# Kernel tuning notes

Measured on AMD Instinct MI355X. Metric: run time of the kernel, lower is better.

Reference implementation:

```python
import jax, jax.numpy as jnp
import numpy as np

N_NODES = 50000
TAU = 1.0 + (1.0 / 1000.0) * (0.1 - 1.0)  # anneal step 1 -> 0.9991


def setup_inputs() -> dict:
    key = jax.random.key(0)
    ks = jax.random.split(key, 8)
    N, F, H, E, K = N_NODES, 128, 128, 800000, 5
    node_features = jax.random.normal(ks[0], (N, F), dtype=jnp.float32)
    src = jnp.sort(jax.random.randint(ks[1], (E,), 0, N, dtype=jnp.int32))
    dst = jax.random.randint(ks[2], (E,), 0, N, dtype=jnp.int32)
    u_noise = jax.random.uniform(ks[3], (K, E), dtype=jnp.float32,
                                 minval=1e-6, maxval=1.0 - 1e-6)
    # MLP params: Linear(2F -> H), ReLU, Linear(H -> 1)
    W1 = jax.random.normal(ks[4], (2 * F, H), dtype=jnp.float32) / np.sqrt(2 * F)
    b1 = jnp.zeros((H,), dtype=jnp.float32)
    W2 = jax.random.normal(ks[5], (H, 1), dtype=jnp.float32) / np.sqrt(H)
    b2 = jnp.zeros((1,), dtype=jnp.float32)
    return {"node_features": node_features, "W1": W1, "b1": b1,
            "W2": W2, "b2": b2, "u_noise": u_noise, "src": src, "dst": dst}


def reference(node_features, W1, b1, W2, b2, u_noise, src, dst):
    N = N_NODES
    F = node_features.shape[1]
    # per-edge MLP on concat([x_u, x_v]) without materializing the (E, 2F) concat
    x_u = node_features[src]                      # (E, F)
    x_v = node_features[dst]                      # (E, F)
    h = jax.nn.relu(x_u @ W1[:F] + x_v @ W1[F:] + b1)   # (E, H)
    z = (h @ W2 + b2)[:, 0]                       # (E,)
    # per-node (segment) log-softmax over each node's neighbor edges
    zmax = jax.ops.segment_max(z, src, num_segments=N)
    ze = z - zmax[src]
    denom = jax.ops.segment_sum(jnp.exp(ze), src, num_segments=N)
    log_pi = ze - jnp.log(denom)[src]             # (E,)
    # k rounds of Gumbel-softmax sampling
    g = -jnp.log(-jnp.log(u_noise))               # (K, E)
    scores = (log_pi[None, :] + g) / TAU          # (K, E)

    def seg_softmax(s):
        m = jax.ops.segment_max(s, src, num_segments=N)
        e = jnp.exp(s - m[src])
        return e / jax.ops.segment_sum(e, src, num_segments=N)[src]

    def seg_argmax_dst(s):
        m = jax.ops.segment_max(s, src, num_segments=N)
        hit = s >= m[src]
        sel = jax.ops.segment_max(jnp.where(hit, dst, -1), src, num_segments=N)
        return sel  # (N,) selected neighbor per node, per round

    soft = jax.vmap(seg_softmax)(scores)          # (K, E) gumbel-softmax probs
    selected = jax.vmap(seg_argmax_dst)(scores)   # (K, N) sampled neighbor ids
    return selected, soft
```

## Files before the change

### kernel.cpp

```cpp
#include <hip/hip_runtime.h>

#define FEAT 128
#define HID  128
#define XS_S 260

__global__ __launch_bounds__(256) void gemm_ab(
    const float* __restrict__ X, const float* __restrict__ W1,
    float* __restrict__ A, float* __restrict__ B, int N) {
  __shared__ float xs[32 * XS_S];
  const int t = threadIdx.x;
  const int lane = t & 63;
  const int n0 = blockIdx.x * 256;
  const int j0 = blockIdx.y * 64;
  const int jj = __builtin_amdgcn_readfirstlane(j0 + (t >> 6) * 16);
  const float* Wp = W1 + (jj < 128 ? jj : 128 * HID + (jj - 128));
  float* Obase = (jj < 128) ? (A + jj) : (B + (jj - 128));

  const int ln = t >> 3;
  const int lf = (t & 7) * 4;

  float acc[4][16];
#pragma unroll
  for (int r = 0; r < 4; ++r)
#pragma unroll
    for (int c = 0; c < 16; ++c) acc[r][c] = 0.f;

  for (int kc = 0; kc < 4; ++kc) {
    __syncthreads();
#pragma unroll
    for (int rep = 0; rep < 8; ++rep) {
      const int nl = ln + rep * 32;
      const int n = n0 + nl;
      float4 v = make_float4(0.f, 0.f, 0.f, 0.f);
      if (n < N) v = *(const float4*)(X + (size_t)n * FEAT + kc * 32 + lf);
      xs[(lf + 0) * XS_S + nl] = v.x;
      xs[(lf + 1) * XS_S + nl] = v.y;
      xs[(lf + 2) * XS_S + nl] = v.z;
      xs[(lf + 3) * XS_S + nl] = v.w;
    }
    __syncthreads();

#pragma unroll 4
    for (int k = 0; k < 32; ++k) {
      const float* wr = Wp + (size_t)(kc * 32 + k) * HID;
      const float4 w0 = *(const float4*)(wr);
      const float4 w1 = *(const float4*)(wr + 4);
      const float4 w2 = *(const float4*)(wr + 8);
      const float4 w3 = *(const float4*)(wr + 12);
      const float4 xv = *(const float4*)&xs[k * XS_S + lane * 4];
      const float xr[4] = {xv.x, xv.y, xv.z, xv.w};
      const float wv[16] = {w0.x, w0.y, w0.z, w0.w, w1.x, w1.y, w1.z, w1.w,
                            w2.x, w2.y, w2.z, w2.w, w3.x, w3.y, w3.z, w3.w};
#pragma unroll
      for (int r = 0; r < 4; ++r)
#pragma unroll
        for (int c = 0; c < 16; ++c)
          acc[r][c] = fmaf(xr[r], wv[c], acc[r][c]);
    }
  }

#pragma unroll
  for (int r = 0; r < 4; ++r) {
    const int n = n0 + lane * 4 + r;
    if (n < N) {
      float* o = Obase + (size_t)n * HID;
#pragma unroll
      for (int c4 = 0; c4 < 4; ++c4)
        *(float4*)(o + c4 * 4) = make_float4(acc[r][c4 * 4 + 0], acc[r][c4 * 4 + 1],
                                             acc[r][c4 * 4 + 2], acc[r][c4 * 4 + 3]);
    }
  }
}

__global__ __launch_bounds__(256) void row_offsets(
    const int* __restrict__ src, int* __restrict__ rs, int N, int E) {
  const int n = blockIdx.x * 256 + threadIdx.x;
  if (n > N) return;
  int lo = 0, hi = E;
  while (lo < hi) {
    const int mid = (lo + hi) >> 1;
    if (src[mid] < n) lo = mid + 1; else hi = mid;
  }
  rs[n] = lo;
}

struct Rows { float4 a0, a1, b0, b1, c0, c1, d0, d1; };

__device__ __forceinline__ void load_pair(
    const float* __restrict__ A, const float* __restrict__ B,
    const int* __restrict__ src, const int* __restrict__ dst,
    int e0, int E, int l, Rows& r) {
  const bool k0 = e0 < E, k1 = e0 + 1 < E;
  const int u0 = k0 ? src[e0] : 0;
  const int v0 = k0 ? dst[e0] : 0;
  const int u1 = k1 ? src[e0 + 1] : 0;
  const int v1 = k1 ? dst[e0 + 1] : 0;
  const float4* Au0 = (const float4*)(A + (size_t)u0 * HID) + l * 2;
  const float4* Bv0 = (const float4*)(B + (size_t)v0 * HID) + l * 2;
  const float4* Au1 = (const float4*)(A + (size_t)u1 * HID) + l * 2;
  const float4* Bv1 = (const float4*)(B + (size_t)v1 * HID) + l * 2;
  r.a0 = Au0[0]; r.a1 = Au0[1];
  r.b0 = Bv0[0]; r.b1 = Bv0[1];
  r.c0 = Au1[0]; r.c1 = Au1[1];
  r.d0 = Bv1[0]; r.d1 = Bv1[1];
}

__global__ __launch_bounds__(256) void edge_z(
    const float* __restrict__ A, const float* __restrict__ B,
    const float* __restrict__ b1, const float* __restrict__ W2,
    const float* __restrict__ b2, const int* __restrict__ src,
    const int* __restrict__ dst, float* __restrict__ z, int E) {
  const int g = threadIdx.x >> 4;
  const int l = threadIdx.x & 15;
  const int base = blockIdx.x * 128 + g * 2;

  const float4 c0 = *(const float4*)(b1 + l * 8);
  const float4 c1 = *(const float4*)(b1 + l * 8 + 4);
  const float4 w0 = *(const float4*)(W2 + l * 8);
  const float4 w1 = *(const float4*)(W2 + l * 8 + 4);
  const float bias2 = b2[0];

  Rows cur, nxt;
  load_pair(A, B, src, dst, base, E, l, cur);

#pragma unroll 4
  for (int it = 0; it < 4; ++it) {
    const int e0 = base + it * 32;
    if (it < 3) load_pair(A, B, src, dst, base + (it + 1) * 32, E, l, nxt);

    float p0 = fmaxf(cur.a0.x + cur.b0.x + c0.x, 0.f) * w0.x
             + fmaxf(cur.a0.y + cur.b0.y + c0.y, 0.f) * w0.y
             + fmaxf(cur.a0.z + cur.b0.z + c0.z, 0.f) * w0.z
             + fmaxf(cur.a0.w + cur.b0.w + c0.w, 0.f) * w0.w
             + fmaxf(cur.a1.x + cur.b1.x + c1.x, 0.f) * w1.x
             + fmaxf(cur.a1.y + cur.b1.y + c1.y, 0.f) * w1.y
             + fmaxf(cur.a1.z + cur.b1.z + c1.z, 0.f) * w1.z
             + fmaxf(cur.a1.w + cur.b1.w + c1.w, 0.f) * w1.w;
    float p1 = fmaxf(cur.c0.x + cur.d0.x + c0.x, 0.f) * w0.x
             + fmaxf(cur.c0.y + cur.d0.y + c0.y, 0.f) * w0.y
             + fmaxf(cur.c0.z + cur.d0.z + c0.z, 0.f) * w0.z
             + fmaxf(cur.c0.w + cur.d0.w + c0.w, 0.f) * w0.w
             + fmaxf(cur.c1.x + cur.d1.x + c1.x, 0.f) * w1.x
             + fmaxf(cur.c1.y + cur.d1.y + c1.y, 0.f) * w1.y
             + fmaxf(cur.c1.z + cur.d1.z + c1.z, 0.f) * w1.z
             + fmaxf(cur.c1.w + cur.d1.w + c1.w, 0.f) * w1.w;

#pragma unroll
    for (int m = 8; m >= 1; m >>= 1) {
      p0 += __shfl_xor(p0, m);
      p1 += __shfl_xor(p1, m);
    }
    if (l == 0 && e0 < E) {
      z[e0] = p0 + bias2;
      if (e0 + 1 < E) z[e0 + 1] = p1 + bias2;
    }
    cur = nxt;
  }
}

__global__ __launch_bounds__(256) void seg_sample(
    const float* __restrict__ z, const float* __restrict__ U,
    const int* __restrict__ dst, const int* __restrict__ rs,
    float* __restrict__ out_sel, float* __restrict__ out_soft,
    int N, int E, int K) {
  const int t = threadIdx.x;
  const int lane = t & 63;
  const int half = lane >> 5;
  const int hl = lane & 31;
  const int n = blockIdx.x * 8 + (t >> 6) * 2 + half;
  const float INVTAU = 1.0f / 0.9991f;

  int start = 0, deg = 0;
  if (n < N) { start = rs[n]; deg = rs[n + 1] - start; }

  if (__all(deg <= 32)) {
    if (n >= N) return;
    if (deg == 0) {
      if (hl == 0)
        for (int k = 0; k < K; ++k) out_sel[(size_t)k * N + n] = -2147483648.0f;
      return;
    }
    const bool act = hl < deg;
    const int e = start + (act ? hl : 0);
    const float zv = act ? z[e] : -INFINITY;
    const int d = act ? dst[e] : -1;

    float zmax = zv;
#pragma unroll
    for (int m = 16; m >= 1; m >>= 1) zmax = fmaxf(zmax, __shfl_xor(zmax, m));
    float den = act ? __expf(zv - zmax) : 0.f;
#pragma unroll
    for (int m = 16; m >= 1; m >>= 1) den += __shfl_xor(den, m);
    const float lpb = (zv - zmax) - __logf(den);

    for (int k = 0; k < K; ++k) {
      float ex = 0.f;
      if (act) {
        const float uu = U[(size_t)k * E + e];
        const float t2 = -__logf(uu);
        const float g = -__logf(t2);
        ex = __expf((lpb + g) * INVTAU);
      }
      float d2 = ex;
      float mx = ex;
      int md = d;
#pragma unroll
      for (int m = 16; m >= 1; m >>= 1) {
        d2 += __shfl_xor(d2, m);
        const float ox = __shfl_xor(mx, m);
        const int od = __shfl_xor(md, m);
        if (ox > mx) { mx = ox; md = od; }
        else if (ox == mx) md = max(md, od);
      }
      if (hl == 0) out_sel[(size_t)k * N + n] = (float)md;
      if (act) {
        const float inv = __builtin_amdgcn_rcpf(d2);
        out_soft[(size_t)k * E + e] = ex * inv;
      }
    }
    return;
  }

  const int wbase = blockIdx.x * 8 + (t >> 6) * 2;
  for (int j = 0; j < 2; ++j) {
    const int nn = wbase + j;
    if (nn >= N) continue;
    const int st = rs[nn];
    const int dg = rs[nn + 1] - st;
    if (dg == 0) {
      if (lane == 0)
        for (int k = 0; k < K; ++k) out_sel[(size_t)k * N + nn] = -2147483648.0f;
      continue;
    }
    float zmax = -INFINITY;
    for (int c = lane; c < dg; c += 64) zmax = fmaxf(zmax, z[st + c]);
#pragma unroll
    for (int m = 32; m >= 1; m >>= 1) zmax = fmaxf(zmax, __shfl_xor(zmax, m));
    float den = 0.f;
    for (int c = lane; c < dg; c += 64) den += expf(z[st + c] - zmax);
#pragma unroll
    for (int m = 32; m >= 1; m >>= 1) den += __shfl_xor(den, m);
    const float logd = logf(den);

    for (int k = 0; k < K; ++k) {
      float m2 = -INFINITY;
      for (int c = lane; c < dg; c += 64) {
        const int e = st + c;
        const float g = -logf(-logf(U[(size_t)k * E + e]));
        const float s = ((z[e] - zmax) - logd + g) * INVTAU;
        m2 = fmaxf(m2, s);
      }
#pragma unroll
      for (int m = 32; m >= 1; m >>= 1) m2 = fmaxf(m2, __shfl_xor(m2, m));
      float d2 = 0.f;
      int cand = -1;
      for (int c = lane; c < dg; c += 64) {
        const int e = st + c;
        const float g = -logf(-logf(U[(size_t)k * E + e]));
        const float s = ((z[e] - zmax) - logd + g) * INVTAU;
        d2 += expf(s - m2);
        if (s >= m2) cand = max(cand, dst[e]);
      }
#pragma unroll
      for (int m = 32; m >= 1; m >>= 1) d2 += __shfl_xor(d2, m);
#pragma unroll
      for (int m = 32; m >= 1; m >>= 1) cand = max(cand, __shfl_xor(cand, m));
      if (lane == 0) out_sel[(size_t)k * N + nn] = (float)cand;
      for (int c = lane; c < dg; c += 64) {
        const int e = st + c;
        const float g = -logf(-logf(U[(size_t)k * E + e]));
        const float s = ((z[e] - zmax) - logd + g) * INVTAU;
        out_soft[(size_t)k * E + e] = expf(s - m2) / d2;
      }
    }
  }
}

extern "C" void kernel_launch(void* const* d_in, const int* in_sizes, int n_in,
                              void* d_out, int out_size, void* d_ws, size_t ws_size,
                              hipStream_t stream) {
  const float* X  = (const float*)d_in[0];
  const float* W1 = (const float*)d_in[1];
  const float* b1 = (const float*)d_in[2];
  const float* W2 = (const float*)d_in[3];
  const float* b2 = (const float*)d_in[4];
  const float* U  = (const float*)d_in[5];
  const int* src  = (const int*)d_in[6];
  const int* dst  = (const int*)d_in[7];
  const int E = in_sizes[6];
  const int K = in_sizes[5] / E;
  const int N = in_sizes[0] / FEAT;

  float* A = (float*)d_ws;
  float* B = A + (size_t)N * HID;
  float* z = B + (size_t)N * HID;
  int* rs  = (int*)(z + E);

  float* out_sel  = (float*)d_out;
  float* out_soft = (float*)d_out + (size_t)K * N;

  hipLaunchKernelGGL(gemm_ab, dim3((N + 255) / 256, 4), dim3(256), 0, stream,
                     X, W1, A, B, N);
  hipLaunchKernelGGL(row_offsets, dim3((N + 256) / 256), dim3(256), 0, stream,
                     src, rs, N, E);
  hipLaunchKernelGGL(edge_z, dim3((E + 127) / 128), dim3(256), 0, stream,
                     A, B, b1, W2, b2, src, dst, z, E);
  hipLaunchKernelGGL(seg_sample, dim3((N + 7) / 8), dim3(256), 0, stream,
                     z, U, dst, rs, out_sel, out_soft, N, E, K);
}
```

Before: 246.0 us.

## Stage W1 tiles in shared memory and compute full 256-column output per block

The node GEMM now has each block cover 128 nodes and all 256 output columns (both the A and B halves) instead of one 64-column slice per block. W1 chunks are staged into padded shared memory rather than read by each wave straight from global memory. Each thread now accumulates an 8x16 register tile instead of 4x16, raising arithmetic intensity, and X is read once rather than four times. In exchange it uses more registers and LDS, which may lower occupancy, and the grid becomes smaller.

```diff
diff --git a/kernel.cpp b/kernel.cpp
--- a/kernel.cpp
+++ b/kernel.cpp
@@ -2,33 +2,40 @@
 
 #define FEAT 128
 #define HID  128
-#define XS_S 260
+#define XS_S 132
+#define WS_S 320
 
 __global__ __launch_bounds__(256) void gemm_ab(
     const float* __restrict__ X, const float* __restrict__ W1,
     float* __restrict__ A, float* __restrict__ B, int N) {
   __shared__ float xs[32 * XS_S];
+  __shared__ float ws[32 * WS_S];
   const int t = threadIdx.x;
+  const int n0 = blockIdx.x * 128;
+
+  const int wave = t >> 6;
+  const int wc = wave & 1;
+  const int wn = wave >> 1;
   const int lane = t & 63;
-  const int n0 = blockIdx.x * 256;
-  const int j0 = blockIdx.y * 64;
-  const int jj = __builtin_amdgcn_readfirstlane(j0 + (t >> 6) * 16);
-  const float* Wp = W1 + (jj < 128 ? jj : 128 * HID + (jj - 128));
-  float* Obase = (jj < 128) ? (A + jj) : (B + (jj - 128));
+  const int ng = lane >> 3;
+  const int cg = lane & 7;
+  const int xbase = wn * 64 + ng * 8;
+  const int cb = wc * 128 + cg * 16;
+  const int woff = cb + ((cb >> 4) << 2);
 
   const int ln = t >> 3;
   const int lf = (t & 7) * 4;
 
-  float acc[4][16];
-#pragma unroll
-  for (int r = 0; r < 4; ++r)
+  float acc[8][16];
+#pragma unroll
+  for (int r = 0; r < 8; ++r)
 #pragma unroll
     for (int c = 0; c < 16; ++c) acc[r][c] = 0.f;
 
   for (int kc = 0; kc < 4; ++kc) {
     __syncthreads();
 #pragma unroll
-    for (int rep = 0; rep < 8; ++rep) {
+    for (int rep = 0; rep < 4; ++rep) {
       const int nl = ln + rep * 32;
       const int n = n0 + nl;
       float4 v = make_float4(0.f, 0.f, 0.f, 0.f);
@@ -38,32 +45,46 @@
       xs[(lf + 2) * XS_S + nl] = v.z;
       xs[(lf + 3) * XS_S + nl] = v.w;
     }
+#pragma unroll
+    for (int rep = 0; rep < 8; ++rep) {
+      const int idx = rep * 256 + t;
+      const int k = idx >> 6;
+      const int jc = (idx & 63) * 4;
+      const float* srcp = (jc < 128)
+          ? W1 + (size_t)(kc * 32 + k) * HID + jc
+          : W1 + (size_t)(128 + kc * 32 + k) * HID + (jc - 128);
+      *(float4*)&ws[k * WS_S + jc + ((jc >> 4) << 2)] = *(const float4*)srcp;
+    }
     __syncthreads();
 
-#pragma unroll 4
+#pragma unroll 2
     for (int k = 0; k < 32; ++k) {
-      const float* wr = Wp + (size_t)(kc * 32 + k) * HID;
+      const float* wr = &ws[k * WS_S + woff];
       const float4 w0 = *(const float4*)(wr);
       const float4 w1 = *(const float4*)(wr + 4);
       const float4 w2 = *(const float4*)(wr + 8);
       const float4 w3 = *(const float4*)(wr + 12);
-      const float4 xv = *(const float4*)&xs[k * XS_S + lane * 4];
-      const float xr[4] = {xv.x, xv.y, xv.z, xv.w};
+      const float* xr = &xs[k * XS_S + xbase];
+      const float4 x0 = *(const float4*)(xr);
+      const float4 x1 = *(const float4*)(xr + 4);
+      const float xv[8] = {x0.x, x0.y, x0.z, x0.w, x1.x, x1.y, x1.z, x1.w};
       const float wv[16] = {w0.x, w0.y, w0.z, w0.w, w1.x, w1.y, w1.z, w1.w,
                             w2.x, w2.y, w2.z, w2.w, w3.x, w3.y, w3.z, w3.w};
 #pragma unroll
-      for (int r = 0; r < 4; ++r)
+      for (int r = 0; r < 8; ++r)
 #pragma unroll
         for (int c = 0; c < 16; ++c)
-          acc[r][c] = fmaf(xr[r], wv[c], acc[r][c]);
-    }
-  }
-
-#pragma unroll
-  for (int r = 0; r < 4; ++r) {
-    const int n = n0 + lane * 4 + r;
+          acc[r][c] = fmaf(xv[r], wv[c], acc[r][c]);
+    }
+  }
+
+  float* Obase = (cb < 128) ? A : B;
+  const int cbm = (cb < 128) ? cb : cb - 128;
+#pragma unroll
+  for (int r = 0; r < 8; ++r) {
+    const int n = n0 + xbase + r;
     if (n < N) {
-      float* o = Obase + (size_t)n * HID;
+      float* o = Obase + (size_t)n * HID + cbm;
 #pragma unroll
       for (int c4 = 0; c4 < 4; ++c4)
         *(float4*)(o + c4 * 4) = make_float4(acc[r][c4 * 4 + 0], acc[r][c4 * 4 + 1],
@@ -299,7 +320,7 @@
   float* out_sel  = (float*)d_out;
   float* out_soft = (float*)d_out + (size_t)K * N;
 
-  hipLaunchKernelGGL(gemm_ab, dim3((N + 255) / 256, 4), dim3(256), 0, stream,
+  hipLaunchKernelGGL(gemm_ab, dim3((N + 127) / 128), dim3(256), 0, stream,
                      X, W1, A, B, N);
   hipLaunchKernelGGL(row_offsets, dim3((N + 256) / 256), dim3(256), 0, stream,
                      src, rs, N, E);
```

Measured after the change: 254.5 us. 3.4% more time.
